# Optimization experiments

Measured on AMD Instinct MI355X. Metric: run time of the kernel, lower is better.

## Reference

```python
import jax, jax.numpy as jnp
import numpy as np

BINARY_K = 64  # self.binary_k


def setup_inputs() -> dict:
    key = jax.random.key(0)
    ks = jax.random.split(key, 8)
    R, N, D, H = 8, 128, 512, 256
    obj_feats = jax.random.normal(ks[0], (R, N, D), dtype=jnp.float32)
    geo_feats = jax.random.normal(ks[1], (R, N, N, D), dtype=jnp.float32) * 0.1
    mask = jnp.ones((N, N), dtype=jnp.float32)
    mask = mask.at[jnp.arange(N), jnp.arange(N)].set(0.0)  # zero diagonal, as in forward()
    s1 = 1.0 / np.sqrt(D)
    s2 = 1.0 / np.sqrt(H)
    return {
        "obj_feats": obj_feats,
        "geo_feats": geo_feats,
        "mask": mask,
        "w1a": jax.random.normal(ks[2], (D, H), dtype=jnp.float32) * s1,
        "b1a": jnp.zeros((H,), dtype=jnp.float32),
        "w2a": jax.random.normal(ks[3], (H, 1), dtype=jnp.float32) * s2,
        "b2a": jnp.zeros((1,), dtype=jnp.float32),
        "w1b": jax.random.normal(ks[4], (D, H), dtype=jnp.float32) * s1,
        "b1b": jnp.zeros((H,), dtype=jnp.float32),
        "w2b": jax.random.normal(ks[5], (H, 1), dtype=jnp.float32) * s2,
        "b2b": jnp.zeros((1,), dtype=jnp.float32),
    }


def reference(obj_feats, geo_feats, mask, w1a, b1a, w2a, b2a, w1b, b1b, w2b, b2b):
    # pair_aware_perbatch (dropout = identity in eval mode)
    R, N, D = obj_feats.shape
    k = min(BINARY_K, N * N)

    # pairwise outer-product features + geometric features: [R, N, N, D]
    obj2obj = obj_feats[:, None, :, :] * obj_feats[:, :, None, :] + geo_feats

    # re_clf1 MLP scorer: D -> D/2 -> 1
    h = jax.nn.relu(jnp.einsum('rijd,dh->rijh', obj2obj, w1a) + b1a)
    logits = jnp.einsum('rijh,h->rij', h, w2a[:, 0]) + b2a[0]     # [R, N, N]
    o2o_logits = logits.reshape(R, N * N).sum(axis=0) / R          # [N*N]

    pair_probs = jax.nn.sigmoid(o2o_logits) * mask.ravel()
    _, topk_inds = jax.lax.top_k(pair_probs, k)                    # [k]

    # averaged pair features, gather topk
    a_obj2obj = obj2obj.reshape(R, N * N, D).sum(axis=0) / R       # [N*N, D]
    pair_feats = a_obj2obj[topk_inds]                              # [k, D]

    # pair-of-pair outer product + second MLP scorer
    p2p = pair_feats[None, :, :] * pair_feats[:, None, :]          # [k, k, D]
    h2 = jax.nn.relu(jnp.einsum('ijd,dh->ijh', p2p, w1b) + b1b)
    p2p_logits = jnp.einsum('ijh,h->ij', h2, w2b[:, 0]) + b2b[0]   # [k, k]

    return o2o_logits.reshape(N, N), p2p_logits, topk_inds
```

## Files before the change

kernel.cpp:

```cpp
#include <hip/hip_runtime.h>
#include <math.h>

typedef unsigned int u32;
typedef unsigned long long u64;
typedef unsigned short u16;
typedef short bf16x8 __attribute__((ext_vector_type(8)));
typedef float f32x4 __attribute__((ext_vector_type(4)));

#define RR 8
#define NN 128
#define DD 512
#define HH 256
#define KTOP 64
#define NCAND 256
#define NSEL 128

#define WS_LOGITS_OFF 0
#define WS_CAND_OFF   65536
#define WS_EXACT_OFF  66560
#define WS_CNT_OFF    67584
#define WS_TOPK_OFF   67600
#define WS_PF_OFF     67856
#define WS_WH_OFF     198928
#define WS_WL_OFF     461072

__device__ __forceinline__ u16 bf16rne(float x) {
    union { float f; u32 u; } v; v.f = x;
    u32 r = (v.u + 0x7fffu + ((v.u >> 16) & 1u)) >> 16;
    return (u16)r;
}
__device__ __forceinline__ float bf16tof(u16 h) {
    union { float f; u32 u; } v; v.u = ((u32)h) << 16; return v.f;
}
__device__ __forceinline__ u32 f32sort(float x) {
    union { float f; u32 u; } v; v.f = x;
    return v.u ^ ((v.u & 0x80000000u) ? 0xFFFFFFFFu : 0x80000000u);
}

__global__ __launch_bounds__(256) void k0_splitW(const float* __restrict__ W1,
                                                 u16* __restrict__ wh, u16* __restrict__ wl)
{
    const int kc = blockIdx.x;
    const int h  = threadIdx.x;
    u16 rh[32], rl[32];
#pragma unroll
    for (int kk = 0; kk < 32; ++kk) {
        float a = W1[(size_t)(kc * 32 + kk) * HH + h];
        u16 hi = bf16rne(a);
        float lo = a - bf16tof(hi);
        rh[kk] = hi; rl[kk] = bf16rne(lo);
    }
    const size_t base = (size_t)kc * 8192 + (size_t)h * 32;
#pragma unroll
    for (int q = 0; q < 4; ++q) {
        uint4 ph, pl;
        ph.x = (u32)rh[q*8+0] | ((u32)rh[q*8+1] << 16);
        ph.y = (u32)rh[q*8+2] | ((u32)rh[q*8+3] << 16);
        ph.z = (u32)rh[q*8+4] | ((u32)rh[q*8+5] << 16);
        ph.w = (u32)rh[q*8+6] | ((u32)rh[q*8+7] << 16);
        pl.x = (u32)rl[q*8+0] | ((u32)rl[q*8+1] << 16);
        pl.y = (u32)rl[q*8+2] | ((u32)rl[q*8+3] << 16);
        pl.z = (u32)rl[q*8+4] | ((u32)rl[q*8+5] << 16);
        pl.w = (u32)rl[q*8+6] | ((u32)rl[q*8+7] << 16);
        *(uint4*)&wh[base + q*8] = ph;
        *(uint4*)&wl[base + q*8] = pl;
    }
}

__global__ __launch_bounds__(256, 2) void k1_pair_mfma(
    const float* __restrict__ obj, const float* __restrict__ geo,
    const u16* __restrict__ wh, const u16* __restrict__ wl,
    const float* __restrict__ b1, const float* __restrict__ w2,
    float* __restrict__ logits_acc)
{
    const int jb = blockIdx.x, i = blockIdx.y, r = blockIdx.z;
    const int j0 = jb * 64;
    const int tid = threadIdx.x;
    const int lane = tid & 63, wv = tid >> 6;
    const int l15 = lane & 15, quad = lane >> 4;

    __shared__ float sObjI[DD];
    __shared__ __align__(16) u16 sAh[64 * 32], sAl[64 * 32];
    __shared__ __align__(16) u16 sBh[256 * 32], sBl[256 * 32];

    const float* objI = obj + (size_t)(r * NN + i) * DD;
    for (int t = tid; t < DD; t += 256) sObjI[t] = objI[t];

    f32x4 acc[4][4];
#pragma unroll
    for (int mt = 0; mt < 4; ++mt)
#pragma unroll
        for (int nt = 0; nt < 4; ++nt) acc[mt][nt] = (f32x4){0.f, 0.f, 0.f, 0.f};

    const float* geoB = geo + ((size_t)(r * NN + i) * NN + j0) * DD;
    const float* objJ = obj + (size_t)(r * NN + j0) * DD;

    const int aj = tid >> 2;
    const int ak = (tid & 3) * 8;

    for (int kc = 0; kc < 16; ++kc) {
        const int k0 = kc * 32;
        __syncthreads();
        {
            const char* gh = (const char*)(wh + (size_t)kc * 8192);
            const char* gl = (const char*)(wl + (size_t)kc * 8192);
#pragma unroll
            for (int p = 0; p < 4; ++p) {
                const int off = (wv * 4 + p) * 1024;
                __builtin_amdgcn_global_load_lds(
                    (const __attribute__((address_space(1))) u32*)(gh + off + lane * 16),
                    (__attribute__((address_space(3))) u32*)((char*)sBh + off), 16, 0, 0);
                __builtin_amdgcn_global_load_lds(
                    (const __attribute__((address_space(1))) u32*)(gl + off + lane * 16),
                    (__attribute__((address_space(3))) u32*)((char*)sBl + off), 16, 0, 0);
            }
        }
        {
            float4 g0 = *(const float4*)(geoB + (size_t)aj * DD + k0 + ak);
            float4 g1 = *(const float4*)(geoB + (size_t)aj * DD + k0 + ak + 4);
            float4 o0 = *(const float4*)(objJ + (size_t)aj * DD + k0 + ak);
            float4 o1 = *(const float4*)(objJ + (size_t)aj * DD + k0 + ak + 4);
            float a[8];
            a[0] = fmaf(sObjI[k0+ak+0], o0.x, g0.x);
            a[1] = fmaf(sObjI[k0+ak+1], o0.y, g0.y);
            a[2] = fmaf(sObjI[k0+ak+2], o0.z, g0.z);
            a[3] = fmaf(sObjI[k0+ak+3], o0.w, g0.w);
            a[4] = fmaf(sObjI[k0+ak+4], o1.x, g1.x);
            a[5] = fmaf(sObjI[k0+ak+5], o1.y, g1.y);
            a[6] = fmaf(sObjI[k0+ak+6], o1.z, g1.z);
            a[7] = fmaf(sObjI[k0+ak+7], o1.w, g1.w);
            u16 hs[8], ls[8];
#pragma unroll
            for (int q = 0; q < 8; ++q) {
                hs[q] = bf16rne(a[q]);
                ls[q] = bf16rne(a[q] - bf16tof(hs[q]));
            }
            uint4 ph, pl;
            ph.x = (u32)hs[0] | ((u32)hs[1] << 16); ph.y = (u32)hs[2] | ((u32)hs[3] << 16);
            ph.z = (u32)hs[4] | ((u32)hs[5] << 16); ph.w = (u32)hs[6] | ((u32)hs[7] << 16);
            pl.x = (u32)ls[0] | ((u32)ls[1] << 16); pl.y = (u32)ls[2] | ((u32)ls[3] << 16);
            pl.z = (u32)ls[4] | ((u32)ls[5] << 16); pl.w = (u32)ls[6] | ((u32)ls[7] << 16);
            *(uint4*)&sAh[aj * 32 + ak] = ph;
            *(uint4*)&sAl[aj * 32 + ak] = pl;
        }
        __syncthreads();
        bf16x8 Bh[4], Bl[4], Ah[4], Al[4];
#pragma unroll
        for (int nt = 0; nt < 4; ++nt) {
            const int row = wv * 64 + nt * 16 + l15;
            Bh[nt] = *(const bf16x8*)&sBh[row * 32 + quad * 8];
            Bl[nt] = *(const bf16x8*)&sBl[row * 32 + quad * 8];
        }
#pragma unroll
        for (int mt = 0; mt < 4; ++mt) {
            const int row = mt * 16 + l15;
            Ah[mt] = *(const bf16x8*)&sAh[row * 32 + quad * 8];
            Al[mt] = *(const bf16x8*)&sAl[row * 32 + quad * 8];
        }
#pragma unroll
        for (int mt = 0; mt < 4; ++mt)
#pragma unroll
            for (int nt = 0; nt < 4; ++nt) {
                acc[mt][nt] = __builtin_amdgcn_mfma_f32_16x16x32_bf16(Ah[mt], Bh[nt], acc[mt][nt], 0, 0, 0);
                acc[mt][nt] = __builtin_amdgcn_mfma_f32_16x16x32_bf16(Ah[mt], Bl[nt], acc[mt][nt], 0, 0, 0);
                acc[mt][nt] = __builtin_amdgcn_mfma_f32_16x16x32_bf16(Al[mt], Bh[nt], acc[mt][nt], 0, 0, 0);
            }
    }
    float pr[4][4];
#pragma unroll
    for (int mt = 0; mt < 4; ++mt)
#pragma unroll
        for (int t = 0; t < 4; ++t) pr[mt][t] = 0.f;
#pragma unroll
    for (int nt = 0; nt < 4; ++nt) {
        const int h = wv * 64 + nt * 16 + l15;
        const float bb = b1[h], w = w2[h];
#pragma unroll
        for (int mt = 0; mt < 4; ++mt)
#pragma unroll
            for (int t = 0; t < 4; ++t)
                pr[mt][t] += fmaxf(acc[mt][nt][t] + bb, 0.f) * w;
    }
#pragma unroll
    for (int mt = 0; mt < 4; ++mt)
#pragma unroll
        for (int t = 0; t < 4; ++t) {
            float v = pr[mt][t];
            v += __shfl_xor(v, 1); v += __shfl_xor(v, 2);
            v += __shfl_xor(v, 4); v += __shfl_xor(v, 8);
            if (l15 == 0)
                atomicAdd(&logits_acc[i * NN + j0 + mt * 16 + quad * 4 + t], v);
        }
}

__global__ __launch_bounds__(1024) void k2_hist(
    const float* __restrict__ logits_acc, const float* __restrict__ mask,
    const float* __restrict__ b2a, float* __restrict__ out,
    int* __restrict__ cand, int* __restrict__ cnt_out)
{
    __shared__ u32 h1[256], h2[256];
    __shared__ int sB1, sRem, sT16;
    __shared__ u32 sCnt;
    const int t = threadIdx.x;
    if (t < 256) { h1[t] = 0; h2[t] = 0; }
    if (t == 0) sCnt = 0;
    __syncthreads();
    const float bias = b2a[0];
    u32 skey[16];
#pragma unroll
    for (int e = 0; e < 16; ++e) {
        const int idx = e * 1024 + t;
        const float lg = logits_acc[idx] * 0.125f + bias;
        out[idx] = lg;
        u32 s = f32sort(lg);
        if (mask[idx] == 0.f) s = 0;
        skey[e] = s;
        atomicAdd(&h1[s >> 24], 1u);
    }
    __syncthreads();
    if (t == 0) {
        u32 cum = 0; int b = 255;
        for (; b > 0; --b) { u32 c = h1[b]; if (cum + c >= (u32)NSEL) break; cum += c; }
        sB1 = b; sRem = NSEL - (int)cum;
    }
    __syncthreads();
    const int B1 = sB1;
#pragma unroll
    for (int e = 0; e < 16; ++e) {
        const u32 s = skey[e];
        if ((int)(s >> 24) == B1) atomicAdd(&h2[(s >> 16) & 0xFF], 1u);
    }
    __syncthreads();
    if (t == 0) {
        const int rem = sRem; u32 cum = 0; int b = 255;
        for (; b > 0; --b) { cum += h2[b]; if ((int)cum >= rem) break; }
        sT16 = (B1 << 8) | b;
    }
    __syncthreads();
    const u32 T16 = (u32)sT16;
#pragma unroll
    for (int e = 0; e < 16; ++e) {
        const u32 s = skey[e];
        if (s != 0 && (s >> 16) >= T16) {
            const u32 pos = atomicAdd(&sCnt, 1u);
            if (pos < (u32)NCAND) cand[pos] = e * 1024 + t;
        }
    }
    __syncthreads();
    if (t == 0) *cnt_out = (int)(sCnt < (u32)NCAND ? sCnt : (u32)NCAND);
}

__global__ __launch_bounds__(256) void k5_exact(
    const float* __restrict__ obj, const float* __restrict__ geo,
    const float* __restrict__ W1, const float* __restrict__ b1,
    const float* __restrict__ w2, const float* __restrict__ b2a,
    const int* __restrict__ cand, const int* __restrict__ cnt_ptr,
    float* __restrict__ exact)
{
    const int c = blockIdx.x;
    if (c >= *cnt_ptr) { if (threadIdx.x == 0) exact[c] = -1e30f; return; }
    const int idx = cand[c];
    const int i = idx >> 7, j = idx & 127;
    const int t = threadIdx.x;
    __shared__ float sA[RR][DD];
    __shared__ float sRed[4];
    for (int f = t; f < RR * DD; f += 256) {
        const int r = f >> 9, k = f & 511;
        sA[r][k] = fmaf(obj[(size_t)(r * NN + i) * DD + k],
                        obj[(size_t)(r * NN + j) * DD + k],
                        geo[((size_t)(r * NN + i) * NN + j) * DD + k]);
    }
    __syncthreads();
    float hv[RR];
#pragma unroll
    for (int r = 0; r < RR; ++r) hv[r] = 0.f;
#pragma unroll 4
    for (int k = 0; k < DD; ++k) {
        const float w = W1[(size_t)k * HH + t];
#pragma unroll
        for (int r = 0; r < RR; ++r) hv[r] = fmaf(sA[r][k], w, hv[r]);
    }
    const float bb = b1[t], wv2 = w2[t];
    float p = 0.f;
#pragma unroll
    for (int r = 0; r < RR; ++r) p += fmaxf(hv[r] + bb, 0.f) * wv2;
#pragma unroll
    for (int off = 1; off < 64; off <<= 1) p += __shfl_xor(p, off);
    if ((t & 63) == 0) sRed[t >> 6] = p;
    __syncthreads();
    if (t == 0) exact[c] = (sRed[0] + sRed[1] + sRed[2] + sRed[3]) * 0.125f + b2a[0];
}

__global__ __launch_bounds__(256) void k_sort(
    const float* __restrict__ exact, const int* __restrict__ cand,
    float* __restrict__ out, int* __restrict__ topk)
{
    __shared__ u64 sKey[NCAND];
    const int t = threadIdx.x;
    {
        const float lg = exact[t];
        u32 ps = 0; u32 idx = 0x7FFFFFFFu;
        if (lg > -1e29f) {
            const float p = 1.f / (1.f + expf(-lg));
            ps = f32sort(p);
            idx = (u32)cand[t];
        }
        sKey[t] = ((u64)ps << 32) | (u64)(0xFFFFFFFFu - idx);
    }
    for (int k = 2; k <= NCAND; k <<= 1)
        for (int j = k >> 1; j > 0; j >>= 1) {
            __syncthreads();
            const int ixj = t ^ j;
            if (ixj > t) {
                const u64 a = sKey[t], b = sKey[ixj];
                if (((t & k) == 0) ? (a < b) : (a > b)) { sKey[t] = b; sKey[ixj] = a; }
            }
        }
    __syncthreads();
    if (t < KTOP) {
        const u32 idx = 0xFFFFFFFFu - (u32)(sKey[t] & 0xFFFFFFFFull);
        topk[t] = (int)idx;
        out[20480 + t] = (float)idx;
    }
}

__global__ __launch_bounds__(256) void k3_gather(
    const float* __restrict__ obj, const float* __restrict__ geo,
    const int* __restrict__ ws_topk, float* __restrict__ pf)
{
    const int tix = blockIdx.x;
    const int idx = ws_topk[tix];
    const int i = idx >> 7, j = idx & 127;
    for (int dd = threadIdx.x; dd < DD; dd += 256) {
        float s = 0.f;
#pragma unroll
        for (int r = 0; r < RR; ++r) {
            const float oi = obj[(size_t)(r * NN + i) * DD + dd];
            const float oj = obj[(size_t)(r * NN + j) * DD + dd];
            const float g  = geo[((size_t)(r * NN + i) * NN + j) * DD + dd];
            s += oi * oj + g;
        }
        pf[tix * DD + dd] = s * 0.125f;
    }
}

__global__ __launch_bounds__(256) void k4_p2p(
    const float* __restrict__ pf, const float* __restrict__ W1,
    const float* __restrict__ b1, const float* __restrict__ w2,
    const float* __restrict__ b2, float* __restrict__ out)
{
    const int a = blockIdx.x;
    const int tid = threadIdx.x;
    const int tx = tid & 15, ty = tid >> 4;

    __shared__ float sPfA[DD];
    __shared__ __align__(16) float sA[32][68];
    __shared__ __align__(16) float sB[32][HH];

    const float* pfA = pf + (size_t)a * DD;
    for (int t = tid; t < DD; t += 256) sPfA[t] = pfA[t];

    float acc[4][16];
#pragma unroll
    for (int m = 0; m < 4; ++m)
#pragma unroll
        for (int n = 0; n < 16; ++n) acc[m][n] = 0.f;

    for (int kc = 0; kc < 16; ++kc) {
        const int k0 = kc * 32;
        __syncthreads();
#pragma unroll
        for (int p = 0; p < 8; ++p) {
            const int f = tid + p * 256;
            const int kk = f >> 6, c = (f & 63) << 2;
            *(float4*)&sB[kk][c] = *(const float4*)&W1[(size_t)(k0 + kk) * HH + c];
        }
#pragma unroll
        for (int p = 0; p < 2; ++p) {
            const int f = tid + p * 256;
            const int j = f >> 3, kk = (f & 7) << 2;
            float4 o = *(const float4*)(pf + (size_t)j * DD + k0 + kk);
            sA[kk + 0][j] = sPfA[k0 + kk + 0] * o.x;
            sA[kk + 1][j] = sPfA[k0 + kk + 1] * o.y;
            sA[kk + 2][j] = sPfA[k0 + kk + 2] * o.z;
            sA[kk + 3][j] = sPfA[k0 + kk + 3] * o.w;
        }
        __syncthreads();
#pragma unroll 8
        for (int kk = 0; kk < 32; ++kk) {
            float4 a4 = *(const float4*)&sA[kk][ty << 2];
            float av[4] = {a4.x, a4.y, a4.z, a4.w};
#pragma unroll
            for (int n4 = 0; n4 < 4; ++n4) {
                float4 b4 = *(const float4*)&sB[kk][(n4 << 6) + (tx << 2)];
                float bv[4] = {b4.x, b4.y, b4.z, b4.w};
#pragma unroll
                for (int m = 0; m < 4; ++m)
#pragma unroll
                    for (int c = 0; c < 4; ++c)
                        acc[m][(n4 << 2) + c] = fmaf(av[m], bv[c], acc[m][(n4 << 2) + c]);
            }
        }
    }
    const float b20 = b2[0];
    float pr[4] = {0.f, 0.f, 0.f, 0.f};
#pragma unroll
    for (int n4 = 0; n4 < 4; ++n4)
#pragma unroll
        for (int c = 0; c < 4; ++c) {
            const int h = (n4 << 6) + (tx << 2) + c;
            const float bb = b1[h], w = w2[h];
#pragma unroll
            for (int m = 0; m < 4; ++m)
                pr[m] += fmaxf(acc[m][(n4 << 2) + c] + bb, 0.f) * w;
        }
#pragma unroll
    for (int m = 0; m < 4; ++m) {
        pr[m] += __shfl_xor(pr[m], 1); pr[m] += __shfl_xor(pr[m], 2);
        pr[m] += __shfl_xor(pr[m], 4); pr[m] += __shfl_xor(pr[m], 8);
        if (tx == 0)
            out[16384 + a * 64 + (ty << 2) + m] = pr[m] + b20;
    }
}

extern "C" void kernel_launch(void* const* d_in, const int* in_sizes, int n_in,
                              void* d_out, int out_size, void* d_ws, size_t ws_size,
                              hipStream_t stream) {
    const float* obj  = (const float*)d_in[0];
    const float* geo  = (const float*)d_in[1];
    const float* mask = (const float*)d_in[2];
    const float* w1a  = (const float*)d_in[3];
    const float* b1a  = (const float*)d_in[4];
    const float* w2a  = (const float*)d_in[5];
    const float* b2a  = (const float*)d_in[6];
    const float* w1b  = (const float*)d_in[7];
    const float* b1b  = (const float*)d_in[8];
    const float* w2b  = (const float*)d_in[9];
    const float* b2b  = (const float*)d_in[10];
    float* out = (float*)d_out;

    char* ws = (char*)d_ws;
    float* ws_logits = (float*)(ws + WS_LOGITS_OFF);
    int*   ws_cand   = (int*)  (ws + WS_CAND_OFF);
    float* ws_exact  = (float*)(ws + WS_EXACT_OFF);
    int*   ws_cnt    = (int*)  (ws + WS_CNT_OFF);
    int*   ws_topk   = (int*)  (ws + WS_TOPK_OFF);
    float* ws_pf     = (float*)(ws + WS_PF_OFF);
    u16*   ws_wh     = (u16*)  (ws + WS_WH_OFF);
    u16*   ws_wl     = (u16*)  (ws + WS_WL_OFF);

    hipMemsetAsync(ws_logits, 0, 16384 * sizeof(float), stream);

    k0_splitW<<<16, 256, 0, stream>>>(w1a, ws_wh, ws_wl);
    k1_pair_mfma<<<dim3(2, NN, RR), 256, 0, stream>>>(obj, geo, ws_wh, ws_wl, b1a, w2a, ws_logits);
    k2_hist<<<1, 1024, 0, stream>>>(ws_logits, mask, b2a, out, ws_cand, ws_cnt);
    k5_exact<<<NCAND, 256, 0, stream>>>(obj, geo, w1a, b1a, w2a, b2a, ws_cand, ws_cnt, ws_exact);
    k_sort<<<1, 256, 0, stream>>>(ws_exact, ws_cand, out, ws_topk);
    k3_gather<<<KTOP, 256, 0, stream>>>(obj, geo, ws_topk, ws_pf);
    k4_p2p<<<KTOP, 256, 0, stream>>>(ws_pf, w1b, b1b, w2b, b2b, out);
}
```

Baseline: 636.8 us.

## Merge j-blocks into 512-thread tiles, swizzle LDS layout, privatize histogram counters

```diff
diff --git a/kernel.cpp b/kernel.cpp
--- a/kernel.cpp
+++ b/kernel.cpp
@@ -42,6 +42,7 @@
 {
     const int kc = blockIdx.x;
     const int h  = threadIdx.x;
+    const int swz = (h >> 1) & 3;
     u16 rh[32], rl[32];
 #pragma unroll
     for (int kk = 0; kk < 32; ++kk) {
@@ -62,29 +63,31 @@
         pl.y = (u32)rl[q*8+2] | ((u32)rl[q*8+3] << 16);
         pl.z = (u32)rl[q*8+4] | ((u32)rl[q*8+5] << 16);
         pl.w = (u32)rl[q*8+6] | ((u32)rl[q*8+7] << 16);
-        *(uint4*)&wh[base + q*8] = ph;
-        *(uint4*)&wl[base + q*8] = pl;
-    }
-}
-
-__global__ __launch_bounds__(256, 2) void k1_pair_mfma(
+        const int qs = (q ^ swz) * 8;
+        *(uint4*)&wh[base + qs] = ph;
+        *(uint4*)&wl[base + qs] = pl;
+    }
+}
+
+__global__ __launch_bounds__(512, 6) void k1_pair_mfma(
     const float* __restrict__ obj, const float* __restrict__ geo,
     const u16* __restrict__ wh, const u16* __restrict__ wl,
     const float* __restrict__ b1, const float* __restrict__ w2,
     float* __restrict__ logits_acc)
 {
-    const int jb = blockIdx.x, i = blockIdx.y, r = blockIdx.z;
-    const int j0 = jb * 64;
+    const int i = blockIdx.x, r = blockIdx.y;
     const int tid = threadIdx.x;
     const int lane = tid & 63, wv = tid >> 6;
     const int l15 = lane & 15, quad = lane >> 4;
+    const int mh = wv >> 2;
+    const int hq = wv & 3;
+    const int fsl = (quad ^ ((l15 >> 1) & 3)) * 8;
 
     __shared__ float sObjI[DD];
-    __shared__ __align__(16) u16 sAh[64 * 32], sAl[64 * 32];
+    __shared__ __align__(16) u16 sAh[128 * 32], sAl[128 * 32];
     __shared__ __align__(16) u16 sBh[256 * 32], sBl[256 * 32];
 
-    const float* objI = obj + (size_t)(r * NN + i) * DD;
-    for (int t = tid; t < DD; t += 256) sObjI[t] = objI[t];
+    sObjI[tid] = obj[(size_t)(r * NN + i) * DD + tid];
 
     f32x4 acc[4][4];
 #pragma unroll
@@ -92,11 +95,12 @@
 #pragma unroll
         for (int nt = 0; nt < 4; ++nt) acc[mt][nt] = (f32x4){0.f, 0.f, 0.f, 0.f};
 
-    const float* geoB = geo + ((size_t)(r * NN + i) * NN + j0) * DD;
-    const float* objJ = obj + (size_t)(r * NN + j0) * DD;
+    const float* geoB = geo + (size_t)(r * NN + i) * NN * DD;
+    const float* objJ = obj + (size_t)r * NN * DD;
 
     const int aj = tid >> 2;
     const int ak = (tid & 3) * 8;
+    const int asl = ((tid & 3) ^ ((aj >> 1) & 3)) * 8;
 
     for (int kc = 0; kc < 16; ++kc) {
         const int k0 = kc * 32;
@@ -105,8 +109,8 @@
             const char* gh = (const char*)(wh + (size_t)kc * 8192);
             const char* gl = (const char*)(wl + (size_t)kc * 8192);
 #pragma unroll
-            for (int p = 0; p < 4; ++p) {
-                const int off = (wv * 4 + p) * 1024;
+            for (int p = 0; p < 2; ++p) {
+                const int off = (wv * 2 + p) * 1024;
                 __builtin_amdgcn_global_load_lds(
                     (const __attribute__((address_space(1))) u32*)(gh + off + lane * 16),
                     (__attribute__((address_space(3))) u32*)((char*)sBh + off), 16, 0, 0);
@@ -140,22 +144,22 @@
             ph.z = (u32)hs[4] | ((u32)hs[5] << 16); ph.w = (u32)hs[6] | ((u32)hs[7] << 16);
             pl.x = (u32)ls[0] | ((u32)ls[1] << 16); pl.y = (u32)ls[2] | ((u32)ls[3] << 16);
             pl.z = (u32)ls[4] | ((u32)ls[5] << 16); pl.w = (u32)ls[6] | ((u32)ls[7] << 16);
-            *(uint4*)&sAh[aj * 32 + ak] = ph;
-            *(uint4*)&sAl[aj * 32 + ak] = pl;
+            *(uint4*)&sAh[aj * 32 + asl] = ph;
+            *(uint4*)&sAl[aj * 32 + asl] = pl;
         }
         __syncthreads();
         bf16x8 Bh[4], Bl[4], Ah[4], Al[4];
 #pragma unroll
         for (int nt = 0; nt < 4; ++nt) {
-            const int row = wv * 64 + nt * 16 + l15;
-            Bh[nt] = *(const bf16x8*)&sBh[row * 32 + quad * 8];
-            Bl[nt] = *(const bf16x8*)&sBl[row * 32 + quad * 8];
+            const int row = hq * 64 + nt * 16 + l15;
+            Bh[nt] = *(const bf16x8*)&sBh[row * 32 + fsl];
+            Bl[nt] = *(const bf16x8*)&sBl[row * 32 + fsl];
         }
 #pragma unroll
         for (int mt = 0; mt < 4; ++mt) {
-            const int row = mt * 16 + l15;
-            Ah[mt] = *(const bf16x8*)&sAh[row * 32 + quad * 8];
-            Al[mt] = *(const bf16x8*)&sAl[row * 32 + quad * 8];
+            const int row = mh * 64 + mt * 16 + l15;
+            Ah[mt] = *(const bf16x8*)&sAh[row * 32 + fsl];
+            Al[mt] = *(const bf16x8*)&sAl[row * 32 + fsl];
         }
 #pragma unroll
         for (int mt = 0; mt < 4; ++mt)
@@ -173,7 +177,7 @@
         for (int t = 0; t < 4; ++t) pr[mt][t] = 0.f;
 #pragma unroll
     for (int nt = 0; nt < 4; ++nt) {
-        const int h = wv * 64 + nt * 16 + l15;
+        const int h = hq * 64 + nt * 16 + l15;
         const float bb = b1[h], w = w2[h];
 #pragma unroll
         for (int mt = 0; mt < 4; ++mt)
@@ -189,7 +193,7 @@
             v += __shfl_xor(v, 1); v += __shfl_xor(v, 2);
             v += __shfl_xor(v, 4); v += __shfl_xor(v, 8);
             if (l15 == 0)
-                atomicAdd(&logits_acc[i * NN + j0 + mt * 16 + quad * 4 + t], v);
+                atomicAdd(&logits_acc[i * NN + mh * 64 + mt * 16 + quad * 4 + t], v);
         }
 }
 
@@ -198,11 +202,13 @@
     const float* __restrict__ b2a, float* __restrict__ out,
     int* __restrict__ cand, int* __restrict__ cnt_out)
 {
-    __shared__ u32 h1[256], h2[256];
+    __shared__ u32 hist[16 * 256];
+    __shared__ u32 sum1[256];
     __shared__ int sB1, sRem, sT16;
     __shared__ u32 sCnt;
     const int t = threadIdx.x;
-    if (t < 256) { h1[t] = 0; h2[t] = 0; }
+    const int hb = (t >> 6) << 8;
+    for (int b = t; b < 16 * 256; b += 1024) hist[b] = 0;
     if (t == 0) sCnt = 0;
     __syncthreads();
     const float bias = b2a[0];
@@ -215,25 +221,41 @@
         u32 s = f32sort(lg);
         if (mask[idx] == 0.f) s = 0;
         skey[e] = s;
-        atomicAdd(&h1[s >> 24], 1u);
+        atomicAdd(&hist[hb + (s >> 24)], 1u);
+    }
+    __syncthreads();
+    if (t < 256) {
+        u32 s = 0;
+#pragma unroll
+        for (int c = 0; c < 16; ++c) s += hist[c * 256 + t];
+        sum1[t] = s;
     }
     __syncthreads();
     if (t == 0) {
         u32 cum = 0; int b = 255;
-        for (; b > 0; --b) { u32 c = h1[b]; if (cum + c >= (u32)NSEL) break; cum += c; }
+        for (; b > 0; --b) { u32 c = sum1[b]; if (cum + c >= (u32)NSEL) break; cum += c; }
         sB1 = b; sRem = NSEL - (int)cum;
     }
     __syncthreads();
     const int B1 = sB1;
+    for (int b = t; b < 16 * 256; b += 1024) hist[b] = 0;
+    __syncthreads();
 #pragma unroll
     for (int e = 0; e < 16; ++e) {
         const u32 s = skey[e];
-        if ((int)(s >> 24) == B1) atomicAdd(&h2[(s >> 16) & 0xFF], 1u);
+        if ((int)(s >> 24) == B1) atomicAdd(&hist[hb + ((s >> 16) & 0xFF)], 1u);
+    }
+    __syncthreads();
+    if (t < 256) {
+        u32 s = 0;
+#pragma unroll
+        for (int c = 0; c < 16; ++c) s += hist[c * 256 + t];
+        sum1[t] = s;
     }
     __syncthreads();
     if (t == 0) {
         const int rem = sRem; u32 cum = 0; int b = 255;
-        for (; b > 0; --b) { cum += h2[b]; if ((int)cum >= rem) break; }
+        for (; b > 0; --b) { cum += sum1[b]; if ((int)cum >= rem) break; }
         sT16 = (B1 << 8) | b;
     }
     __syncthreads();
@@ -452,7 +474,7 @@
     hipMemsetAsync(ws_logits, 0, 16384 * sizeof(float), stream);
 
     k0_splitW<<<16, 256, 0, stream>>>(w1a, ws_wh, ws_wl);
-    k1_pair_mfma<<<dim3(2, NN, RR), 256, 0, stream>>>(obj, geo, ws_wh, ws_wl, b1a, w2a, ws_logits);
+    k1_pair_mfma<<<dim3(NN, RR), 512, 0, stream>>>(obj, geo, ws_wh, ws_wl, b1a, w2a, ws_logits);
     k2_hist<<<1, 1024, 0, stream>>>(ws_logits, mask, b2a, out, ws_cand, ws_cnt);
     k5_exact<<<NCAND, 256, 0, stream>>>(obj, geo, w1a, b1a, w2a, b2a, ws_cand, ws_cnt, ws_exact);
     k_sort<<<1, 256, 0, stream>>>(ws_exact, ws_cand, out, ws_topk);
```

New measurement: 1.334 ms. +109.5%, slower.
